# Optimization experiments

Hardware: AMD Instinct MI355X
Metric: run time of the kernel (lower is better)

Reference implementation:

```python
import jax, jax.numpy as jnp
import numpy as np

B = 262144   # number of coordinates (512x512 grid)
O = 256      # out_features
D = 2        # in_features (coordinate dim)
ALPHA = 6.0


def setup_inputs() -> dict:
    key = jax.random.key(0)
    k_x, k_w, k_b, k_mu, k_g = jax.random.split(key, 5)
    x = jax.random.uniform(k_x, (B, D), jnp.float32, -1.0, 1.0)      # coordinates in [-1,1]^D
    W = jax.random.normal(k_w, (O, D), jnp.float32)                   # quantized-freq weights (frozen)
    b = jax.random.uniform(k_b, (O,), jnp.float32, -np.pi, np.pi)     # phase
    mu = jax.random.uniform(k_mu, (1, O, D), jnp.float32, -1.0, 1.0)  # Gaussian centers
    gamma = jax.random.gamma(k_g, ALPHA, (O,), jnp.float32)           # Gamma(alpha, 1) bandwidths
    return {"x": x, "W": W, "b": b, "mu": mu, "gamma": gamma}


def reference(x, W, b, mu, gamma):
    # linear: (B, O)
    lin = x @ W.T + b
    # squared distance to per-output centers: broadcast (B,1,D) - (1,O,D) -> sum over D
    dist2 = jnp.sum((x[:, None, :] - mu) ** 2, axis=-1)  # (B, O)
    return jnp.sin(lin) * jnp.exp(-0.5 * dist2 * gamma[None, :])
```

## Files before the change

### kernel.cpp

```cpp
#include <hip/hip_runtime.h>


#define NROWS 262144
#define NOUT  256

__global__ __launch_bounds__(256, 4)
void gabor_kernel(const float* __restrict__ x,
                  const float* __restrict__ W,
                  const float* __restrict__ b,
                  const float* __restrict__ mu,
                  const float* __restrict__ gamma,
                  float* __restrict__ out,
                  int rows_per_block)
{
    const int tid  = threadIdx.x;
    const int oq   = (tid & 63) * 4;
    const int rsub = tid >> 6;

    float W0[4], W1[4], bb[4], mu0[4], mu1[4], ng[4];
#pragma unroll
    for (int j = 0; j < 4; ++j) {
        const int o = oq + j;
        W0[j]  = W[o * 2 + 0];
        W1[j]  = W[o * 2 + 1];
        bb[j]  = b[o];
        mu0[j] = mu[o * 2 + 0];
        mu1[j] = mu[o * 2 + 1];
        ng[j]  = -0.5f * gamma[o];
    }

    const int row_base = blockIdx.x * rows_per_block;
#pragma unroll 2
    for (int r = rsub; r < rows_per_block; r += 4) {
        const int i = row_base + r;
        const float2 xv = *reinterpret_cast<const float2*>(x + (size_t)i * 2);

        float4 res;
        float* rp = &res.x;
#pragma unroll
        for (int j = 0; j < 4; ++j) {
            const float lin = __fmaf_rn(xv.x, W0[j], __fmaf_rn(xv.y, W1[j], bb[j]));
            const float dx  = xv.x - mu0[j];
            const float dy  = xv.y - mu1[j];
            const float d2  = __fmaf_rn(dy, dy, dx * dx);
            rp[j] = __sinf(lin) * __expf(d2 * ng[j]);
        }
        *reinterpret_cast<float4*>(out + (size_t)i * NOUT + oq) = res;
    }
}

extern "C" void kernel_launch(void* const* d_in, const int* in_sizes, int n_in,
                              void* d_out, int out_size, void* d_ws, size_t ws_size,
                              hipStream_t stream)
{
    const float* x     = (const float*)d_in[0];
    const float* W     = (const float*)d_in[1];
    const float* b     = (const float*)d_in[2];
    const float* mu    = (const float*)d_in[3];
    const float* gamma = (const float*)d_in[4];
    float* out = (float*)d_out;

    const int rows_per_block = 64;
    const int grid = NROWS / rows_per_block;
    gabor_kernel<<<grid, 256, 0, stream>>>(x, W, b, mu, gamma, out, rows_per_block);
}
```

Baseline: 268.4 us.

## Use hardware sin/exp2 with prescaled constants, 4 rows per thread, nontemporal stores

Prescales weights and bias by 1/(2π) so the raw hardware sine builtin can be used, and folds log2(e) into the gamma coefficient to use exp2 directly. Each thread now handles 4 rows per iteration with wider x loads, and the output is written with nontemporal stores to avoid polluting the cache. Rows per block double. Relies on the hardware sine's limited input range and precision.

```diff
diff --git a/kernel.cpp b/kernel.cpp
--- a/kernel.cpp
+++ b/kernel.cpp
@@ -3,6 +3,17 @@
 
 #define NROWS 262144
 #define NOUT  256
+#define RPB   128
+#define INV2PI 0.15915494309189535f
+#define LOG2E  1.4426950408889634f
+
+typedef float v4f __attribute__((ext_vector_type(4)));
+
+#if __has_builtin(__builtin_amdgcn_exp2f)
+#define EXP2F(v) __builtin_amdgcn_exp2f(v)
+#else
+#define EXP2F(v) exp2f(v)
+#endif
 
 __global__ __launch_bounds__(256, 4)
 void gabor_kernel(const float* __restrict__ x,
@@ -10,42 +21,56 @@
                   const float* __restrict__ b,
                   const float* __restrict__ mu,
                   const float* __restrict__ gamma,
-                  float* __restrict__ out,
-                  int rows_per_block)
+                  float* __restrict__ out)
 {
     const int tid  = threadIdx.x;
     const int oq   = (tid & 63) * 4;
-    const int rsub = tid >> 6;
+    const int wsub = tid >> 6;
 
     float W0[4], W1[4], bb[4], mu0[4], mu1[4], ng[4];
 #pragma unroll
     for (int j = 0; j < 4; ++j) {
         const int o = oq + j;
-        W0[j]  = W[o * 2 + 0];
-        W1[j]  = W[o * 2 + 1];
-        bb[j]  = b[o];
+        W0[j]  = W[o * 2 + 0] * INV2PI;
+        W1[j]  = W[o * 2 + 1] * INV2PI;
+        bb[j]  = b[o] * INV2PI;
         mu0[j] = mu[o * 2 + 0];
         mu1[j] = mu[o * 2 + 1];
-        ng[j]  = -0.5f * gamma[o];
+        ng[j]  = -0.5f * LOG2E * gamma[o];
     }
 
-    const int row_base = blockIdx.x * rows_per_block;
+    const int row0 = blockIdx.x * RPB + wsub * 4;
+    const float4* xv = reinterpret_cast<const float4*>(x);
+
 #pragma unroll 2
-    for (int r = rsub; r < rows_per_block; r += 4) {
-        const int i = row_base + r;
-        const float2 xv = *reinterpret_cast<const float2*>(x + (size_t)i * 2);
+    for (int it = 0; it < RPB / 16; ++it) {
+        const int r = row0 + it * 16;
+        const float4 xa = xv[(r >> 1) + 0];
+        const float4 xb = xv[(r >> 1) + 1];
 
-        float4 res;
-        float* rp = &res.x;
+        const float px[4] = {xa.x, xa.z, xb.x, xb.z};
+        const float py[4] = {xa.y, xa.w, xb.y, xb.w};
+
+        v4f res[4];
 #pragma unroll
-        for (int j = 0; j < 4; ++j) {
-            const float lin = __fmaf_rn(xv.x, W0[j], __fmaf_rn(xv.y, W1[j], bb[j]));
-            const float dx  = xv.x - mu0[j];
-            const float dy  = xv.y - mu1[j];
-            const float d2  = __fmaf_rn(dy, dy, dx * dx);
-            rp[j] = __sinf(lin) * __expf(d2 * ng[j]);
+        for (int rr = 0; rr < 4; ++rr) {
+#pragma unroll
+            for (int j = 0; j < 4; ++j) {
+                const float lin = __fmaf_rn(px[rr], W0[j],
+                                  __fmaf_rn(py[rr], W1[j], bb[j]));
+                const float dx  = px[rr] - mu0[j];
+                const float dy  = py[rr] - mu1[j];
+                const float d2  = __fmaf_rn(dy, dy, dx * dx);
+                res[rr][j] = __builtin_amdgcn_sinf(lin) * EXP2F(d2 * ng[j]);
+            }
         }
-        *reinterpret_cast<float4*>(out + (size_t)i * NOUT + oq) = res;
+
+        float* orow = out + (size_t)r * NOUT + oq;
+#pragma unroll
+        for (int rr = 0; rr < 4; ++rr) {
+            __builtin_nontemporal_store(res[rr],
+                reinterpret_cast<v4f*>(orow + rr * NOUT));
+        }
     }
 }
 
@@ -60,7 +85,6 @@
     const float* gamma = (const float*)d_in[4];
     float* out = (float*)d_out;
 
-    const int rows_per_block = 64;
-    const int grid = NROWS / rows_per_block;
-    gabor_kernel<<<grid, 256, 0, stream>>>(x, W, b, mu, gamma, out, rows_per_block);
+    const int grid = NROWS / RPB;
+    gabor_kernel<<<grid, 256, 0, stream>>>(x, W, b, mu, gamma, out);
 }
```

Measured after the change: 280.8 us. +4.6%, slower.
